# Kernel optimization log

Hardware: AMD Instinct MI355X
Metric: run time of the kernel (lower is better)

## Reference

```python
import jax, jax.numpy as jnp
import numpy as np

B, T, D, E, C = 4, 4096, 2048, 8, 1024
H = D // E  # per-expert hidden = out_features // num_experts = 256


def setup_inputs() -> dict:
    key = jax.random.key(0)
    ks = jax.random.split(key, 7)
    x = jax.random.normal(ks[0], (B, T, D), dtype=jnp.float32)
    # nn.Linear-style init scale ~ 1/sqrt(fan_in)
    W1 = jax.random.normal(ks[1], (E, H, D), dtype=jnp.float32) / np.sqrt(D)
    b1 = jax.random.normal(ks[2], (E, H), dtype=jnp.float32) / np.sqrt(D)
    W2 = jax.random.normal(ks[3], (E, D, H), dtype=jnp.float32) / np.sqrt(D)
    b2 = jax.random.normal(ks[4], (D,), dtype=jnp.float32) / np.sqrt(D)
    expert_indices = jax.random.randint(ks[5], (B, E, C), 0, T, dtype=jnp.int32)
    expert_gate = jax.random.uniform(ks[6], (B, E, C), dtype=jnp.float32)
    return {"x": x, "W1": W1, "b1": b1, "W2": W2, "b2": b2,
            "expert_indices": expert_indices, "expert_gate": expert_gate,
            "num_tokens": T}


def reference(x, W1, b1, W2, b2, expert_indices, expert_gate, num_tokens):
    # x: (B,T,D); expert_indices/expert_gate: (B,E,C)
    Bb = x.shape[0]
    Ee, Cc = expert_indices.shape[1], expert_indices.shape[2]
    b_idx = jnp.arange(Bb)[:, None, None]
    # dispatch: gather tokens per expert -> (B,E,C,D)
    sel = x[b_idx, expert_indices]
    # contract: per-expert GEMM -> (B,E,C,H)
    h = jnp.einsum('becd,ehd->bech', sel, W1) + b1[None, :, None, :]
    h = jax.nn.gelu(h, approximate=False)
    # expand: per-expert GEMM -> (B,E,C,D), shared output bias
    y = jnp.einsum('bech,eoh->beco', h, W2) + b2
    y = y * expert_gate[..., None]
    # combine: gated scatter-add back to token positions -> (B,T,D)
    out = jnp.zeros((Bb, num_tokens, x.shape[2]), dtype=x.dtype)
    out = out.at[jnp.arange(Bb)[:, None], expert_indices.reshape(Bb, Ee * Cc)].add(
        y.reshape(Bb, Ee * Cc, -1))
    return out
```

## Files before the change

kernel.cpp:

```cpp
#include <hip/hip_runtime.h>
#include <hip/hip_bf16.h>
#include <math.h>

#define B_ 4
#define T_ 4096
#define D_ 2048
#define E_ 8
#define C_ 1024
#define H_ 256
#define SLOTCAP 32

typedef unsigned short u16;
typedef unsigned long long u64;
typedef __attribute__((ext_vector_type(8))) short short8;
typedef __attribute__((ext_vector_type(4))) float f32x4;

__device__ __forceinline__ u16 f2bf(float f) {
    union { float f; unsigned u; } v; v.f = f;
    unsigned r = (v.u + 0x7FFFu + ((v.u >> 16) & 1u)) >> 16;
    return (u16)r;
}
__device__ __forceinline__ u16 f2bf_n(float f) {
    union { __hip_bfloat16 b; u16 u; } v;
    v.b = __float2bfloat16(f);
    return v.u;
}
__device__ __forceinline__ float bf2f(u16 u) {
    union { unsigned u; float f; } v; v.u = ((unsigned)u) << 16;
    return v.f;
}

__device__ __forceinline__ int swz(int row, int chunk) {
    return (row << 6) + ((chunk ^ (row & 7)) << 3);
}

__global__ __launch_bounds__(256) void conv_f32_bf16(
    const float* __restrict__ src, u16* __restrict__ dst, int n)
{
    int i = (blockIdx.x * 256 + threadIdx.x) * 4;
    if (i >= n) return;
    f32x4 v = *reinterpret_cast<const f32x4*>(src + i);
    u16 o[4];
    o[0] = f2bf(v[0]); o[1] = f2bf(v[1]); o[2] = f2bf(v[2]); o[3] = f2bf(v[3]);
    *reinterpret_cast<u64*>(dst + i) = *reinterpret_cast<const u64*>(o);
}

__global__ __launch_bounds__(512) void gemm1_v5(
    const float* __restrict__ x, const u16* __restrict__ W1bf,
    const float* __restrict__ b1, const int* __restrict__ idx,
    u16* __restrict__ Hbuf)
{
    const int mt = blockIdx.x;
    const int be = blockIdx.y;
    const int b = be >> 3, e = be & 7;
    const int m0 = mt * 128;

    __shared__ __align__(16) u16 As[2][128 * 64];
    __shared__ __align__(16) u16 Bs[2][256 * 64];
    __shared__ int toks[128];
    __shared__ float bs1[256];

    const int tid = threadIdx.x;
    if (tid < 128) toks[tid] = idx[(b * E_ + e) * C_ + m0 + tid];
    if (tid < 256) bs1[tid] = b1[e * H_ + tid];
    __syncthreads();

    const int lane = tid & 63, wid = tid >> 6;
    const int wm = wid >> 2, wn = wid & 3;
    const int l15 = lane & 15, lk = lane >> 4;

    const int ar = tid >> 2, ac0 = tid & 3;
    const float* aRow = x + (size_t)b * (T_ * (size_t)D_)
                          + (size_t)toks[ar] * D_;
    const int br = tid >> 1, bc0 = (tid & 1) * 4;
    const u16* bRow = W1bf + ((size_t)e * H_ + br) * D_;

    const int aOff0 = swz(ar, ac0), aOff1 = swz(ar, ac0 + 4);
    int bOff[4];
    #pragma unroll
    for (int j = 0; j < 4; ++j) bOff[j] = swz(br, bc0 + j);

    f32x4 acc[4][4];
    #pragma unroll
    for (int i = 0; i < 4; ++i)
        #pragma unroll
        for (int j = 0; j < 4; ++j)
            acc[i][j] = (f32x4){0.f, 0.f, 0.f, 0.f};

    f32x4 pa[4];
    short8 pb[4];

#define G1_LOAD(k)                                                            \
    do {                                                                      \
        pa[0] = *reinterpret_cast<const f32x4*>(aRow + (k) + ac0 * 8);        \
        pa[1] = *reinterpret_cast<const f32x4*>(aRow + (k) + ac0 * 8 + 4);    \
        pa[2] = *reinterpret_cast<const f32x4*>(aRow + (k) + (ac0 + 4) * 8);  \
        pa[3] = *reinterpret_cast<const f32x4*>(aRow + (k) + (ac0 + 4) * 8 + 4);\
        _Pragma("unroll")                                                     \
        for (int j = 0; j < 4; ++j)                                           \
            pb[j] = *reinterpret_cast<const short8*>(bRow + (k) + (bc0 + j) * 8);\
    } while (0)

#define G1_WRITE(buf)                                                         \
    do {                                                                      \
        short8 s0, s1;                                                        \
        _Pragma("unroll")                                                     \
        for (int r = 0; r < 4; ++r) {                                         \
            s0[r] = (short)f2bf_n(pa[0][r]); s0[r + 4] = (short)f2bf_n(pa[1][r]); \
            s1[r] = (short)f2bf_n(pa[2][r]); s1[r + 4] = (short)f2bf_n(pa[3][r]); \
        }                                                                     \
        *reinterpret_cast<short8*>(&As[buf][aOff0]) = s0;                     \
        *reinterpret_cast<short8*>(&As[buf][aOff1]) = s1;                     \
        _Pragma("unroll")                                                     \
        for (int j = 0; j < 4; ++j)                                           \
            *reinterpret_cast<short8*>(&Bs[buf][bOff[j]]) = pb[j];            \
    } while (0)

    G1_LOAD(0);
    G1_WRITE(0);
    G1_LOAD(64);
    asm volatile("s_waitcnt lgkmcnt(0)" ::: "memory");
    __builtin_amdgcn_s_barrier();

    const int NT = D_ / 64;
    for (int t = 0; t < NT; ++t) {
        const int cur = t & 1;
        if (t + 1 < NT) G1_WRITE(cur ^ 1);
        if (t + 2 < NT) G1_LOAD((t + 2) * 64);
        #pragma unroll
        for (int kk = 0; kk < 2; ++kk) {
            short8 af[4], bfr[4];
            #pragma unroll
            for (int m = 0; m < 4; ++m) {
                const int row = wm * 64 + m * 16 + l15;
                af[m] = *reinterpret_cast<const short8*>(
                    &As[cur][swz(row, kk * 4 + lk)]);
            }
            #pragma unroll
            for (int n = 0; n < 4; ++n) {
                const int row = wn * 64 + n * 16 + l15;
                bfr[n] = *reinterpret_cast<const short8*>(
                    &Bs[cur][swz(row, kk * 4 + lk)]);
            }
            __builtin_amdgcn_s_setprio(1);
            #pragma unroll
            for (int m = 0; m < 4; ++m)
                #pragma unroll
                for (int n = 0; n < 4; ++n)
                    acc[m][n] = __builtin_amdgcn_mfma_f32_16x16x32_bf16(
                        bfr[n], af[m], acc[m][n], 0, 0, 0);
            __builtin_amdgcn_s_setprio(0);
        }
        asm volatile("s_waitcnt lgkmcnt(0)" ::: "memory");
        __builtin_amdgcn_s_barrier();
    }
#undef G1_LOAD
#undef G1_WRITE

    const size_t hbase = ((size_t)(b * E_ + e) * C_ + m0) * H_;
    #pragma unroll
    for (int m = 0; m < 4; ++m) {
        const int cl = wm * 64 + m * 16 + l15;
        u16* rowp = Hbuf + hbase + (size_t)cl * H_;
        #pragma unroll
        for (int n = 0; n < 4; ++n) {
            const int hb = wn * 64 + n * 16 + lk * 4;
            u16 o[4];
            #pragma unroll
            for (int r = 0; r < 4; ++r) {
                float h = acc[m][n][r] + bs1[hb + r];
                float g = 0.5f * h * (1.0f + erff(h * 0.70710678118f));
                o[r] = f2bf_n(g);
            }
            *reinterpret_cast<u64*>(rowp + hb) = *reinterpret_cast<const u64*>(o);
        }
    }
}

__global__ __launch_bounds__(512) void gemm2_v3(
    const u16* __restrict__ Hbuf, const u16* __restrict__ W2bf,
    const float* __restrict__ b2, const float* __restrict__ gate,
    u16* __restrict__ Ybuf)
{
    const int mt = blockIdx.x >> 3, nt = blockIdx.x & 7;
    const int be = blockIdx.y;
    const int b = be >> 3, e = be & 7;
    const int m0 = mt * 128, n0 = nt * 256;

    __shared__ __align__(16) u16 As[2][128 * 64];
    __shared__ __align__(16) u16 Bs[2][256 * 64];
    __shared__ float gs[128];
    __shared__ float bs2[256];

    const int tid = threadIdx.x;
    if (tid < 128) gs[tid] = gate[(b * E_ + e) * C_ + m0 + tid];
    if (tid < 256) bs2[tid] = b2[n0 + tid];
    __syncthreads();

    const int lane = tid & 63, wid = tid >> 6;
    const int wm = wid >> 2, wn = wid & 3;
    const int l15 = lane & 15, lk = lane >> 4;

    const int ar = tid >> 2, ac0 = tid & 3;
    const u16* aRow = Hbuf + ((size_t)(b * E_ + e) * C_ + m0 + ar) * H_;
    const int br = tid >> 1, bc0 = (tid & 1) * 4;
    const u16* bRow = W2bf + ((size_t)e * D_ + n0 + br) * H_;

    const int aOff0 = swz(ar, ac0), aOff1 = swz(ar, ac0 + 4);
    int bOff[4];
    #pragma unroll
    for (int j = 0; j < 4; ++j) bOff[j] = swz(br, bc0 + j);

    f32x4 acc[4][4];
    #pragma unroll
    for (int i = 0; i < 4; ++i)
        #pragma unroll
        for (int j = 0; j < 4; ++j)
            acc[i][j] = (f32x4){0.f, 0.f, 0.f, 0.f};

    short8 pa0, pa1, pb[4];

#define G2_LOAD(k)                                                            \
    do {                                                                      \
        pa0 = *reinterpret_cast<const short8*>(aRow + (k) + ac0 * 8);         \
        pa1 = *reinterpret_cast<const short8*>(aRow + (k) + (ac0 + 4) * 8);   \
        _Pragma("unroll")                                                     \
        for (int j = 0; j < 4; ++j)                                           \
            pb[j] = *reinterpret_cast<const short8*>(bRow + (k) + (bc0 + j) * 8);\
    } while (0)

#define G2_WRITE(buf)                                                         \
    do {                                                                      \
        *reinterpret_cast<short8*>(&As[buf][aOff0]) = pa0;                    \
        *reinterpret_cast<short8*>(&As[buf][aOff1]) = pa1;                    \
        _Pragma("unroll")                                                     \
        for (int j = 0; j < 4; ++j)                                           \
            *reinterpret_cast<short8*>(&Bs[buf][bOff[j]]) = pb[j];            \
    } while (0)

    G2_LOAD(0);
    G2_WRITE(0);
    G2_LOAD(64);
    asm volatile("s_waitcnt lgkmcnt(0)" ::: "memory");
    __builtin_amdgcn_s_barrier();

    const int NT = H_ / 64;
    for (int t = 0; t < NT; ++t) {
        const int cur = t & 1;
        if (t + 1 < NT) G2_WRITE(cur ^ 1);
        if (t + 2 < NT) G2_LOAD((t + 2) * 64);
        #pragma unroll
        for (int kk = 0; kk < 2; ++kk) {
            short8 af[4], bfr[4];
            #pragma unroll
            for (int m = 0; m < 4; ++m) {
                const int row = wm * 64 + m * 16 + l15;
                af[m] = *reinterpret_cast<const short8*>(
                    &As[cur][swz(row, kk * 4 + lk)]);
            }
            #pragma unroll
            for (int n = 0; n < 4; ++n) {
                const int row = wn * 64 + n * 16 + l15;
                bfr[n] = *reinterpret_cast<const short8*>(
                    &Bs[cur][swz(row, kk * 4 + lk)]);
            }
            __builtin_amdgcn_s_setprio(1);
            #pragma unroll
            for (int m = 0; m < 4; ++m)
                #pragma unroll
                for (int n = 0; n < 4; ++n)
                    acc[m][n] = __builtin_amdgcn_mfma_f32_16x16x32_bf16(
                        bfr[n], af[m], acc[m][n], 0, 0, 0);
            __builtin_amdgcn_s_setprio(0);
        }
        asm volatile("s_waitcnt lgkmcnt(0)" ::: "memory");
        __builtin_amdgcn_s_barrier();
    }
#undef G2_LOAD
#undef G2_WRITE

    const size_t ybase = (size_t)(b * E_ + e) * C_ + m0;
    #pragma unroll
    for (int m = 0; m < 4; ++m) {
        const int cl = wm * 64 + m * 16 + l15;
        const float g = gs[cl];
        u16* rowp = Ybuf + (ybase + cl) * (size_t)D_ + n0;
        #pragma unroll
        for (int n = 0; n < 4; ++n) {
            const int db = wn * 64 + n * 16 + lk * 4;
            u16 o[4];
            #pragma unroll
            for (int r = 0; r < 4; ++r)
                o[r] = f2bf_n((acc[m][n][r] + bs2[db + r]) * g);
            *reinterpret_cast<u64*>(rowp + db) = *reinterpret_cast<const u64*>(o);
        }
    }
}

__global__ __launch_bounds__(256) void fill_kernel(
    const int* __restrict__ idx, int* __restrict__ cnt,
    int* __restrict__ slots)
{
    int i = blockIdx.x * 256 + threadIdx.x;
    if (i >= B_ * E_ * C_) return;
    int b = i / (E_ * C_);
    int slot = i % (E_ * C_);
    int t = idx[i];
    int p = atomicAdd(&cnt[b * T_ + t], 1);
    if (p < SLOTCAP) slots[(b * T_ + t) * SLOTCAP + p] = slot;
}

__global__ __launch_bounds__(256) void combine_kernel(
    const u16* __restrict__ Ybuf, const int* __restrict__ cnt,
    const int* __restrict__ slots, float* __restrict__ out)
{
    const int bt = blockIdx.x;
    const int tid = threadIdx.x;
    __shared__ int sl[SLOTCAP];
    int n = cnt[bt];
    n = n > SLOTCAP ? SLOTCAP : n;
    if (tid < n) sl[tid] = slots[bt * SLOTCAP + tid];
    __syncthreads();
    const int b = bt >> 12;
    float a[8] = {0.f, 0.f, 0.f, 0.f, 0.f, 0.f, 0.f, 0.f};
    for (int s = 0; s < n; ++s) {
        const u16* yrow = Ybuf + ((size_t)b * (E_ * C_) + sl[s]) * D_ + tid * 8;
        short8 v = *reinterpret_cast<const short8*>(yrow);
        #pragma unroll
        for (int j = 0; j < 8; ++j) a[j] += bf2f((u16)v[j]);
    }
    float* orow = out + (size_t)bt * D_ + tid * 8;
    *reinterpret_cast<f32x4*>(orow)     = (f32x4){a[0], a[1], a[2], a[3]};
    *reinterpret_cast<f32x4*>(orow + 4) = (f32x4){a[4], a[5], a[6], a[7]};
}

extern "C" void kernel_launch(void* const* d_in, const int* in_sizes, int n_in,
                              void* d_out, int out_size, void* d_ws, size_t ws_size,
                              hipStream_t stream) {
    const float* x    = (const float*)d_in[0];
    const float* W1   = (const float*)d_in[1];
    const float* b1   = (const float*)d_in[2];
    const float* W2   = (const float*)d_in[3];
    const float* b2   = (const float*)d_in[4];
    const int*   idx  = (const int*)d_in[5];
    const float* gate = (const float*)d_in[6];
    float* out = (float*)d_out;

    const size_t nW = (size_t)E_ * H_ * D_;
    const size_t nH = (size_t)B_ * E_ * C_ * H_;
    const size_t nY = (size_t)B_ * E_ * C_ * D_;

    u16* W1bf = (u16*)d_ws;
    u16* W2bf = W1bf + nW;
    u16* Hbuf = W2bf + nW;
    u16* Ybuf = Hbuf + nH;
    int* cnt   = (int*)(Ybuf + nY);
    int* slots = cnt + (size_t)B_ * T_;

    hipMemsetAsync(cnt, 0, (size_t)B_ * T_ * sizeof(int), stream);
    conv_f32_bf16<<<(int)(nW / 1024), 256, 0, stream>>>(W1, W1bf, (int)nW);
    conv_f32_bf16<<<(int)(nW / 1024), 256, 0, stream>>>(W2, W2bf, (int)nW);
    fill_kernel<<<(B_ * E_ * C_) / 256, 256, 0, stream>>>(idx, cnt, slots);

    gemm1_v5<<<dim3(8, 32), 512, 0, stream>>>(x, W1bf, b1, idx, Hbuf);
    gemm2_v3<<<dim3(64, 32), 512, 0, stream>>>(Hbuf, W2bf, b2, gate, Ybuf);
    combine_kernel<<<B_ * T_, 256, 0, stream>>>(Ybuf, cnt, slots, out);
}
```

Before: 231.1 us.

## Stage GEMM tiles via direct global-to-LDS loads from pre-swizzled bf16 images

Weights are converted once into pre-swizzled, tile-contiguous bf16 images. x is pre-converted to bf16 in a separate pass, and gemm1 writes H in the same tiled-swizzled layout. Both GEMMs then replace the register-staged load/convert/LDS-write pipeline with global_load_lds DMA into double-buffered shared memory, synchronised by vmcnt waits. The goal is to remove VGPR staging, in-loop conversion and LDS write instructions from the main loop. The cost is an extra full pass over x (converting 128MB of fp32 to bf16) and added layout complexity, with xbf aliasing Ybuf.

Result: slower. 244.5 us (+5.8%).

```diff
diff --git a/kernel.cpp b/kernel.cpp
--- a/kernel.cpp
+++ b/kernel.cpp
@@ -15,11 +15,6 @@
 typedef __attribute__((ext_vector_type(8))) short short8;
 typedef __attribute__((ext_vector_type(4))) float f32x4;
 
-__device__ __forceinline__ u16 f2bf(float f) {
-    union { float f; unsigned u; } v; v.f = f;
-    unsigned r = (v.u + 0x7FFFu + ((v.u >> 16) & 1u)) >> 16;
-    return (u16)r;
-}
 __device__ __forceinline__ u16 f2bf_n(float f) {
     union { __hip_bfloat16 b; u16 u; } v;
     v.b = __float2bfloat16(f);
@@ -34,29 +29,74 @@
     return (row << 6) + ((chunk ^ (row & 7)) << 3);
 }
 
-__global__ __launch_bounds__(256) void conv_f32_bf16(
+__device__ __forceinline__ void gload16(const void* g, void* l) {
+    __builtin_amdgcn_global_load_lds(
+        (const __attribute__((address_space(1))) void*)g,
+        (__attribute__((address_space(3))) void*)l, 16, 0, 0);
+}
+
+__global__ __launch_bounds__(256) void conv_x_bf16(
     const float* __restrict__ src, u16* __restrict__ dst, int n)
 {
     int i = (blockIdx.x * 256 + threadIdx.x) * 4;
     if (i >= n) return;
     f32x4 v = *reinterpret_cast<const f32x4*>(src + i);
     u16 o[4];
-    o[0] = f2bf(v[0]); o[1] = f2bf(v[1]); o[2] = f2bf(v[2]); o[3] = f2bf(v[3]);
+    o[0] = f2bf_n(v[0]); o[1] = f2bf_n(v[1]); o[2] = f2bf_n(v[2]); o[3] = f2bf_n(v[3]);
     *reinterpret_cast<u64*>(dst + i) = *reinterpret_cast<const u64*>(o);
 }
 
-__global__ __launch_bounds__(512) void gemm1_v5(
-    const float* __restrict__ x, const u16* __restrict__ W1bf,
+__global__ __launch_bounds__(256) void conv_w1_img(
+    const float* __restrict__ W1, u16* __restrict__ img)
+{
+    const int cid = blockIdx.x * 256 + threadIdx.x;
+    const int e = cid >> 16;
+    const int kt = (cid >> 11) & 31;
+    const int row = (cid >> 3) & 255;
+    const int sc = cid & 7;
+    const float* s = W1 + (((size_t)e * 256 + row) * 2048 + kt * 64
+                           + ((sc ^ (row & 7)) << 3));
+    f32x4 v0 = *reinterpret_cast<const f32x4*>(s);
+    f32x4 v1 = *reinterpret_cast<const f32x4*>(s + 4);
+    u16 o[8];
+    #pragma unroll
+    for (int j = 0; j < 4; ++j) { o[j] = f2bf_n(v0[j]); o[j + 4] = f2bf_n(v1[j]); }
+    *reinterpret_cast<short8*>(img + (size_t)cid * 8) =
+        *reinterpret_cast<const short8*>(o);
+}
+
+__global__ __launch_bounds__(256) void conv_w2_img(
+    const float* __restrict__ W2, u16* __restrict__ img)
+{
+    const int cid = blockIdx.x * 256 + threadIdx.x;
+    const int e = cid >> 16;
+    const int nt = (cid >> 13) & 7;
+    const int kt = (cid >> 11) & 3;
+    const int row = (cid >> 3) & 255;
+    const int sc = cid & 7;
+    const float* s = W2 + (((size_t)e * 2048 + nt * 256 + row) * 256 + kt * 64
+                           + ((sc ^ (row & 7)) << 3));
+    f32x4 v0 = *reinterpret_cast<const f32x4*>(s);
+    f32x4 v1 = *reinterpret_cast<const f32x4*>(s + 4);
+    u16 o[8];
+    #pragma unroll
+    for (int j = 0; j < 4; ++j) { o[j] = f2bf_n(v0[j]); o[j + 4] = f2bf_n(v1[j]); }
+    *reinterpret_cast<short8*>(img + (size_t)cid * 8) =
+        *reinterpret_cast<const short8*>(o);
+}
+
+__global__ __launch_bounds__(512) void gemm1_v6(
+    const u16* __restrict__ xbf, const u16* __restrict__ W1img,
     const float* __restrict__ b1, const int* __restrict__ idx,
-    u16* __restrict__ Hbuf)
+    u16* __restrict__ Himg)
 {
     const int mt = blockIdx.x;
     const int be = blockIdx.y;
     const int b = be >> 3, e = be & 7;
     const int m0 = mt * 128;
 
-    __shared__ __align__(16) u16 As[2][128 * 64];
-    __shared__ __align__(16) u16 Bs[2][256 * 64];
+    __shared__ __align__(16) u16 As[2][8192];
+    __shared__ __align__(16) u16 Bs[2][16384];
     __shared__ int toks[128];
     __shared__ float bs1[256];
 
@@ -69,16 +109,26 @@
     const int wm = wid >> 2, wn = wid & 3;
     const int l15 = lane & 15, lk = lane >> 4;
 
-    const int ar = tid >> 2, ac0 = tid & 3;
-    const float* aRow = x + (size_t)b * (T_ * (size_t)D_)
-                          + (size_t)toks[ar] * D_;
-    const int br = tid >> 1, bc0 = (tid & 1) * 4;
-    const u16* bRow = W1bf + ((size_t)e * H_ + br) * D_;
-
-    const int aOff0 = swz(ar, ac0), aOff1 = swz(ar, ac0 + 4);
-    int bOff[4];
-    #pragma unroll
-    for (int j = 0; j < 4; ++j) bOff[j] = swz(br, bc0 + j);
+    const int s0 = tid;
+    const int arow0 = s0 >> 3, asc = s0 & 7;
+    const int arow1 = arow0 + 64;
+    const u16* aSrc0 = xbf + ((size_t)b * T_ + toks[arow0]) * D_
+                           + ((asc ^ (arow0 & 7)) << 3);
+    const u16* aSrc1 = xbf + ((size_t)b * T_ + toks[arow1]) * D_
+                           + ((asc ^ (arow1 & 7)) << 3);
+    const u16* bSrc = W1img + (size_t)e * 32 * 16384 + (size_t)s0 * 8;
+    const int ldsb = wid * 512;
+
+#define G1_ISSUE(buf, kt)                                                     \
+    do {                                                                      \
+        const u16* b_ = bSrc + (size_t)(kt) * 16384;                          \
+        gload16(aSrc0 + (kt) * 64, &As[buf][ldsb]);                           \
+        gload16(aSrc1 + (kt) * 64, &As[buf][4096 + ldsb]);                    \
+        gload16(b_,                &Bs[buf][ldsb]);                           \
+        gload16(b_ + 4096,         &Bs[buf][4096 + ldsb]);                    \
+        gload16(b_ + 8192,         &Bs[buf][8192 + ldsb]);                    \
+        gload16(b_ + 12288,        &Bs[buf][12288 + ldsb]);                   \
+    } while (0)
 
     f32x4 acc[4][4];
     #pragma unroll
@@ -87,46 +137,16 @@
         for (int j = 0; j < 4; ++j)
             acc[i][j] = (f32x4){0.f, 0.f, 0.f, 0.f};
 
-    f32x4 pa[4];
-    short8 pb[4];
-
-#define G1_LOAD(k)                                                            \
-    do {                                                                      \
-        pa[0] = *reinterpret_cast<const f32x4*>(aRow + (k) + ac0 * 8);        \
-        pa[1] = *reinterpret_cast<const f32x4*>(aRow + (k) + ac0 * 8 + 4);    \
-        pa[2] = *reinterpret_cast<const f32x4*>(aRow + (k) + (ac0 + 4) * 8);  \
-        pa[3] = *reinterpret_cast<const f32x4*>(aRow + (k) + (ac0 + 4) * 8 + 4);\
-        _Pragma("unroll")                                                     \
-        for (int j = 0; j < 4; ++j)                                           \
-            pb[j] = *reinterpret_cast<const short8*>(bRow + (k) + (bc0 + j) * 8);\
-    } while (0)
-
-#define G1_WRITE(buf)                                                         \
-    do {                                                                      \
-        short8 s0, s1;                                                        \
-        _Pragma("unroll")                                                     \
-        for (int r = 0; r < 4; ++r) {                                         \
-            s0[r] = (short)f2bf_n(pa[0][r]); s0[r + 4] = (short)f2bf_n(pa[1][r]); \
-            s1[r] = (short)f2bf_n(pa[2][r]); s1[r + 4] = (short)f2bf_n(pa[3][r]); \
-        }                                                                     \
-        *reinterpret_cast<short8*>(&As[buf][aOff0]) = s0;                     \
-        *reinterpret_cast<short8*>(&As[buf][aOff1]) = s1;                     \
-        _Pragma("unroll")                                                     \
-        for (int j = 0; j < 4; ++j)                                           \
-            *reinterpret_cast<short8*>(&Bs[buf][bOff[j]]) = pb[j];            \
-    } while (0)
-
-    G1_LOAD(0);
-    G1_WRITE(0);
-    G1_LOAD(64);
-    asm volatile("s_waitcnt lgkmcnt(0)" ::: "memory");
-    __builtin_amdgcn_s_barrier();
+    G1_ISSUE(0, 0);
+    G1_ISSUE(1, 1);
 
     const int NT = D_ / 64;
     for (int t = 0; t < NT; ++t) {
         const int cur = t & 1;
-        if (t + 1 < NT) G1_WRITE(cur ^ 1);
-        if (t + 2 < NT) G1_LOAD((t + 2) * 64);
+        if (t < NT - 1) asm volatile("s_waitcnt vmcnt(6)" ::: "memory");
+        else            asm volatile("s_waitcnt vmcnt(0)" ::: "memory");
+        __builtin_amdgcn_s_barrier();
+        __builtin_amdgcn_sched_barrier(0);
         #pragma unroll
         for (int kk = 0; kk < 2; ++kk) {
             short8 af[4], bfr[4];
@@ -153,15 +173,15 @@
         }
         asm volatile("s_waitcnt lgkmcnt(0)" ::: "memory");
         __builtin_amdgcn_s_barrier();
-    }
-#undef G1_LOAD
-#undef G1_WRITE
-
-    const size_t hbase = ((size_t)(b * E_ + e) * C_ + m0) * H_;
+        __builtin_amdgcn_sched_barrier(0);
+        if (t + 2 < NT) G1_ISSUE(cur, t + 2);
+    }
+#undef G1_ISSUE
+
+    const size_t hblk = ((size_t)(be * 8 + mt) * 4 + wn) * 8192;
     #pragma unroll
     for (int m = 0; m < 4; ++m) {
-        const int cl = wm * 64 + m * 16 + l15;
-        u16* rowp = Hbuf + hbase + (size_t)cl * H_;
+        const int row = wm * 64 + m * 16 + l15;
         #pragma unroll
         for (int n = 0; n < 4; ++n) {
             const int hb = wn * 64 + n * 16 + lk * 4;
@@ -172,13 +192,15 @@
                 float g = 0.5f * h * (1.0f + erff(h * 0.70710678118f));
                 o[r] = f2bf_n(g);
             }
-            *reinterpret_cast<u64*>(rowp + hb) = *reinterpret_cast<const u64*>(o);
+            const int lc = (n * 2 + (lk >> 1)) ^ (row & 7);
+            u16* p = Himg + hblk + row * 64 + lc * 8 + (lk & 1) * 4;
+            *reinterpret_cast<u64*>(p) = *reinterpret_cast<const u64*>(o);
         }
     }
 }
 
-__global__ __launch_bounds__(512) void gemm2_v3(
-    const u16* __restrict__ Hbuf, const u16* __restrict__ W2bf,
+__global__ __launch_bounds__(512) void gemm2_v4(
+    const u16* __restrict__ Himg, const u16* __restrict__ W2img,
     const float* __restrict__ b2, const float* __restrict__ gate,
     u16* __restrict__ Ybuf)
 {
@@ -187,8 +209,8 @@
     const int b = be >> 3, e = be & 7;
     const int m0 = mt * 128, n0 = nt * 256;
 
-    __shared__ __align__(16) u16 As[2][128 * 64];
-    __shared__ __align__(16) u16 Bs[2][256 * 64];
+    __shared__ __align__(16) u16 As[2][8192];
+    __shared__ __align__(16) u16 Bs[2][16384];
     __shared__ float gs[128];
     __shared__ float bs2[256];
 
@@ -201,15 +223,22 @@
     const int wm = wid >> 2, wn = wid & 3;
     const int l15 = lane & 15, lk = lane >> 4;
 
-    const int ar = tid >> 2, ac0 = tid & 3;
-    const u16* aRow = Hbuf + ((size_t)(b * E_ + e) * C_ + m0 + ar) * H_;
-    const int br = tid >> 1, bc0 = (tid & 1) * 4;
-    const u16* bRow = W2bf + ((size_t)e * D_ + n0 + br) * H_;
-
-    const int aOff0 = swz(ar, ac0), aOff1 = swz(ar, ac0 + 4);
-    int bOff[4];
-    #pragma unroll
-    for (int j = 0; j < 4; ++j) bOff[j] = swz(br, bc0 + j);
+    const int s0 = tid;
+    const u16* aSrc = Himg + ((size_t)(be * 8 + mt) * 4) * 8192 + (size_t)s0 * 8;
+    const u16* bSrc = W2img + ((size_t)(e * 8 + nt) * 4) * 16384 + (size_t)s0 * 8;
+    const int ldsb = wid * 512;
+
+#define G2_ISSUE(buf, kt)                                                     \
+    do {                                                                      \
+        const u16* a_ = aSrc + (size_t)(kt) * 8192;                           \
+        const u16* b_ = bSrc + (size_t)(kt) * 16384;                          \
+        gload16(a_,         &As[buf][ldsb]);                                  \
+        gload16(a_ + 4096,  &As[buf][4096 + ldsb]);                           \
+        gload16(b_,         &Bs[buf][ldsb]);                                  \
+        gload16(b_ + 4096,  &Bs[buf][4096 + ldsb]);                           \
+        gload16(b_ + 8192,  &Bs[buf][8192 + ldsb]);                           \
+        gload16(b_ + 12288, &Bs[buf][12288 + ldsb]);                          \
+    } while (0)
 
     f32x4 acc[4][4];
     #pragma unroll
@@ -218,37 +247,16 @@
         for (int j = 0; j < 4; ++j)
             acc[i][j] = (f32x4){0.f, 0.f, 0.f, 0.f};
 
-    short8 pa0, pa1, pb[4];
-
-#define G2_LOAD(k)                                                            \
-    do {                                                                      \
-        pa0 = *reinterpret_cast<const short8*>(aRow + (k) + ac0 * 8);         \
-        pa1 = *reinterpret_cast<const short8*>(aRow + (k) + (ac0 + 4) * 8);   \
-        _Pragma("unroll")                                                     \
-        for (int j = 0; j < 4; ++j)                                           \
-            pb[j] = *reinterpret_cast<const short8*>(bRow + (k) + (bc0 + j) * 8);\
-    } while (0)
-
-#define G2_WRITE(buf)                                                         \
-    do {                                                                      \
-        *reinterpret_cast<short8*>(&As[buf][aOff0]) = pa0;                    \
-        *reinterpret_cast<short8*>(&As[buf][aOff1]) = pa1;                    \
-        _Pragma("unroll")                                                     \
-        for (int j = 0; j < 4; ++j)                                           \
-            *reinterpret_cast<short8*>(&Bs[buf][bOff[j]]) = pb[j];            \
-    } while (0)
-
-    G2_LOAD(0);
-    G2_WRITE(0);
-    G2_LOAD(64);
-    asm volatile("s_waitcnt lgkmcnt(0)" ::: "memory");
-    __builtin_amdgcn_s_barrier();
+    G2_ISSUE(0, 0);
+    G2_ISSUE(1, 1);
 
     const int NT = H_ / 64;
     for (int t = 0; t < NT; ++t) {
         const int cur = t & 1;
-        if (t + 1 < NT) G2_WRITE(cur ^ 1);
-        if (t + 2 < NT) G2_LOAD((t + 2) * 64);
+        if (t < NT - 1) asm volatile("s_waitcnt vmcnt(6)" ::: "memory");
+        else            asm volatile("s_waitcnt vmcnt(0)" ::: "memory");
+        __builtin_amdgcn_s_barrier();
+        __builtin_amdgcn_sched_barrier(0);
         #pragma unroll
         for (int kk = 0; kk < 2; ++kk) {
             short8 af[4], bfr[4];
@@ -275,9 +283,10 @@
         }
         asm volatile("s_waitcnt lgkmcnt(0)" ::: "memory");
         __builtin_amdgcn_s_barrier();
-    }
-#undef G2_LOAD
-#undef G2_WRITE
+        __builtin_amdgcn_sched_barrier(0);
+        if (t + 2 < NT) G2_ISSUE(cur, t + 2);
+    }
+#undef G2_ISSUE
 
     const size_t ybase = (size_t)(b * E_ + e) * C_ + m0;
     #pragma unroll
@@ -347,22 +356,25 @@
     float* out = (float*)d_out;
 
     const size_t nW = (size_t)E_ * H_ * D_;
+    const size_t nX = (size_t)B_ * T_ * D_;
     const size_t nH = (size_t)B_ * E_ * C_ * H_;
     const size_t nY = (size_t)B_ * E_ * C_ * D_;
 
-    u16* W1bf = (u16*)d_ws;
-    u16* W2bf = W1bf + nW;
-    u16* Hbuf = W2bf + nW;
-    u16* Ybuf = Hbuf + nH;
+    u16* W1img = (u16*)d_ws;
+    u16* W2img = W1img + nW;
+    u16* Himg  = W2img + nW;
+    u16* Ybuf  = Himg + nH;
+    u16* xbf   = Ybuf;
     int* cnt   = (int*)(Ybuf + nY);
     int* slots = cnt + (size_t)B_ * T_;
 
     hipMemsetAsync(cnt, 0, (size_t)B_ * T_ * sizeof(int), stream);
-    conv_f32_bf16<<<(int)(nW / 1024), 256, 0, stream>>>(W1, W1bf, (int)nW);
-    conv_f32_bf16<<<(int)(nW / 1024), 256, 0, stream>>>(W2, W2bf, (int)nW);
+    conv_w1_img<<<2048, 256, 0, stream>>>(W1, W1img);
+    conv_w2_img<<<2048, 256, 0, stream>>>(W2, W2img);
+    conv_x_bf16<<<(int)(nX / 1024), 256, 0, stream>>>(x, xbf, (int)nX);
     fill_kernel<<<(B_ * E_ * C_) / 256, 256, 0, stream>>>(idx, cnt, slots);
 
-    gemm1_v5<<<dim3(8, 32), 512, 0, stream>>>(x, W1bf, b1, idx, Hbuf);
-    gemm2_v3<<<dim3(64, 32), 512, 0, stream>>>(Hbuf, W2bf, b2, gate, Ybuf);
+    gemm1_v6<<<dim3(8, 32), 512, 0, stream>>>(xbf, W1img, b1, idx, Himg);
+    gemm2_v4<<<dim3(64, 32), 512, 0, stream>>>(Himg, W2img, b2, gate, Ybuf);
     combine_kernel<<<B_ * T_, 256, 0, stream>>>(Ybuf, cnt, slots, out);
 }
```
